# Performance work log

Measured on AMD Instinct MI355X. Metric: run time of the kernel, lower is better.

## Reference

```python
import jax, jax.numpy as jnp
import numpy as np

K = 3          # kernel size
STRIDE = 1
PAD = 1
GROUPS = 32    # GroupNorm groups
EPS = 1e-5


def setup_inputs() -> dict:
    key = jax.random.key(0)
    ks = jax.random.split(key, 6)
    B, Cin, H, W, Cout = 4, 256, 64, 64, 256
    K2 = K * K
    x = jax.random.normal(ks[0], (B, Cin, H, W), jnp.float32)
    offset = jax.random.normal(ks[1], (B, 2 * K2, H, W), jnp.float32)
    mask = jax.random.uniform(ks[2], (B, K2, H, W), jnp.float32)
    weight = jax.random.normal(ks[3], (Cout, Cin, K, K), jnp.float32) * (1.0 / np.sqrt(Cin * K2))
    bias = jnp.zeros((Cout,), jnp.float32)
    gamma = jnp.ones((Cout,), jnp.float32)   # constant_init(norm, 1)
    beta = jnp.zeros((Cout,), jnp.float32)   # bias=0
    return {"x": x, "offset": offset, "mask": mask, "weight": weight,
            "bias": bias, "gamma": gamma, "beta": beta}


def _modulated_deform_conv(x, offset, mask, weight, bias):
    """DCNv2: bilinear-sample x at learned offsets, modulate by mask, conv-accumulate."""
    B, Cin, H, W = x.shape
    Cout = weight.shape[0]
    K2 = K * K
    Ho = (H + 2 * PAD - K) // STRIDE + 1
    Wo = (W + 2 * PAD - K) // STRIDE + 1

    # base sampling grid per kernel point: [K2, Ho, Wo]
    ky, kx = jnp.meshgrid(jnp.arange(K), jnp.arange(K), indexing='ij')
    ky = ky.reshape(K2).astype(jnp.float32)
    kx = kx.reshape(K2).astype(jnp.float32)
    hs = (jnp.arange(Ho) * STRIDE - PAD).astype(jnp.float32)
    ws = (jnp.arange(Wo) * STRIDE - PAD).astype(jnp.float32)

    off = offset.reshape(B, K2, 2, Ho, Wo)  # interleaved (dy, dx) per kernel point
    y = ky[None, :, None, None] + hs[None, None, :, None] + off[:, :, 0]   # [B,K2,Ho,Wo]
    xc = kx[None, :, None, None] + ws[None, None, None, :] + off[:, :, 1]  # [B,K2,Ho,Wo]

    y0 = jnp.floor(y)
    x0 = jnp.floor(xc)
    dy = y - y0
    dx = xc - x0
    y0i = y0.astype(jnp.int32)
    x0i = x0.astype(jnp.int32)

    x_flat = x.reshape(B, Cin, H * W)

    def corner(yi, xi, w):
        # corner-wise zero padding outside the image (matches mmcv bilinear)
        valid = (yi >= 0) & (yi <= H - 1) & (xi >= 0) & (xi <= W - 1)
        idx = jnp.clip(yi, 0, H - 1) * W + jnp.clip(xi, 0, W - 1)  # [B,K2,Ho,Wo]
        idx_f = idx.reshape(B, -1)
        v = jax.vmap(lambda xf, i: xf[:, i])(x_flat, idx_f)  # [B, Cin, K2*Ho*Wo]
        wv = (w * valid.astype(w.dtype)).reshape(B, 1, -1)
        return v * wv

    val = (corner(y0i,     x0i,     (1 - dy) * (1 - dx))
         + corner(y0i,     x0i + 1, (1 - dy) * dx)
         + corner(y0i + 1, x0i,     dy * (1 - dx))
         + corner(y0i + 1, x0i + 1, dy * dx))
    val = val.reshape(B, Cin, K2, Ho, Wo) * mask[:, None]  # modulate

    w_r = weight.reshape(Cout, Cin, K2)
    out = jnp.einsum('bckhw,ock->bohw', val, w_r) + bias[None, :, None, None]
    return out


def _group_norm(x, gamma, beta):
    B, C, H, W = x.shape
    g = x.reshape(B, GROUPS, C // GROUPS, H, W)
    mu = g.mean(axis=(2, 3, 4), keepdims=True)
    var = ((g - mu) ** 2).mean(axis=(2, 3, 4), keepdims=True)
    g = (g - mu) * jax.lax.rsqrt(var + EPS)
    return g.reshape(B, C, H, W) * gamma[None, :, None, None] + beta[None, :, None, None]


def reference(x, offset, mask, weight, bias, gamma, beta):
    out = _modulated_deform_conv(x, offset, mask, weight, bias)
    out = _group_norm(out, gamma, beta)
    return jax.nn.relu(out)
```

## Files before the change

kernel.cpp:

```cpp
#include <hip/hip_runtime.h>
#include <math.h>

#define BB    4
#define CIN   256
#define HH    64
#define WWID  64
#define COUT  256
#define KKS   3
#define K2    9
#define PADV  1
#define HWSZ  4096
#define GROUPS 32
#define CPG   8
#define EPSV  1e-5f
#define ROWB  4608
#define NKC   36

typedef __attribute__((ext_vector_type(8))) short bf16x8;
typedef __attribute__((ext_vector_type(4))) float f32x4;

#define GLOAD_LDS16(g, l) \
    __builtin_amdgcn_global_load_lds((const __attribute__((address_space(1))) unsigned int*)(g), \
                                     (__attribute__((address_space(3))) unsigned int*)(l), 16, 0, 0)

__device__ __forceinline__ unsigned short f2bf(float f) {
    unsigned u = __float_as_uint(f);
    u = (u + 0x7fffu + ((u >> 16) & 1u)) >> 16;
    return (unsigned short)u;
}
__device__ __forceinline__ float bflo(unsigned q) { return __uint_as_float(q << 16); }
__device__ __forceinline__ float bfhi(unsigned q) { return __uint_as_float(q & 0xffff0000u); }
__device__ __forceinline__ void fma8(float* f, float w, uint4 q) {
    f[0] += w * bflo(q.x); f[1] += w * bfhi(q.x);
    f[2] += w * bflo(q.y); f[3] += w * bfhi(q.y);
    f[4] += w * bflo(q.z); f[5] += w * bfhi(q.z);
    f[6] += w * bflo(q.w); f[7] += w * bfhi(q.w);
}

__global__ __launch_bounds__(256)
void k_pre(const float* __restrict__ x, unsigned short* __restrict__ xh,
           const float* __restrict__ w, unsigned short* __restrict__ wtb,
           float* __restrict__ gstat) {
    int t = threadIdx.x;
    if (blockIdx.x < 128) {
        __shared__ float tile[32][33];
        int hw0 = blockIdx.x * 32;
        int c0  = blockIdx.y * 32;
        int b   = blockIdx.z;
        int tx = t & 31, ty = t >> 5;
        const float* xp = x + (size_t)b * CIN * HWSZ;
        #pragma unroll
        for (int i = 0; i < 4; i++)
            tile[ty + i * 8][tx] = xp[(c0 + ty + i * 8) * HWSZ + hw0 + tx];
        __syncthreads();
        int j = t >> 3, cq = t & 7;
        union { unsigned short s[4]; uint2 d; } pk;
        #pragma unroll
        for (int k = 0; k < 4; k++) pk.s[k] = f2bf(tile[cq * 4 + k][j]);
        *(uint2*)((char*)xh + ((size_t)b * HWSZ * CIN + (size_t)(hw0 + j) * CIN + c0 + cq * 4) * 2) = pk.d;
    } else {
        if (blockIdx.y == 0 && blockIdx.z == 0)
            for (int i = t; i < BB * GROUPS * 2 + 8; i += 256) gstat[i] = 0.f;
        int idx = (blockIdx.y * 4 + blockIdx.z) * 256 + t;
        int co = idx >> 5, c8 = idx & 31;
        int cin0 = c8 * 8;
        int q = c8 >> 3, c = c8 & 7;
        int pc = c ^ (co & 7);
        for (int k2 = 0; k2 < K2; k2++) {
            union { unsigned short s[8]; uint4 qq; } pk;
            #pragma unroll
            for (int j = 0; j < 8; j++)
                pk.s[j] = f2bf(w[(co * CIN + cin0 + j) * K2 + k2]);
            int phys = co * ROWB + k2 * 512 + q * 128 + pc * 16;
            *(uint4*)((char*)wtb + phys) = pk.qq;
        }
    }
}

__global__ __launch_bounds__(256)
void k_conv(const unsigned short* __restrict__ wtb, const unsigned short* __restrict__ xh,
            const float* __restrict__ offset, const float* __restrict__ mask,
            const float* __restrict__ bias, float* __restrict__ out,
            float* __restrict__ gstat) {
    __shared__ unsigned short As[128 * 64];
    __shared__ unsigned short Bs[64 * 64];
    __shared__ int   cidx[64 * K2 * 4];
    __shared__ float cwgt[64 * K2 * 4];
    __shared__ float gs[16], gss[16];

    int lid = blockIdx.x;
    int j8  = lid >> 3;
    int mt  = j8 & 1;
    int strip = (lid & 7) * 32 + (j8 >> 1);
    int b = strip >> 6;
    int hwbase = (strip & 63) * 64;
    int m0 = mt * 128;

    int t = threadIdx.x, w = t >> 6, l = t & 63;
    int r16 = l & 15, half = l >> 4;
    int wm = w & 1, wn = w >> 1;
    int skey = r16 & 7;

    if (t < 16) { gs[t] = 0.f; gss[t] = 0.f; }

    for (int i = t; i < 64 * K2; i += 256) {
        int px = i / K2, k2 = i - px * K2;
        int hw = hwbase + px;
        int ho = hw >> 6, wo = hw & 63;
        int ky = k2 / KKS, kx = k2 - ky * KKS;
        float dy = offset[((b * (2 * K2) + k2 * 2 + 0) * HWSZ) + hw];
        float dx = offset[((b * (2 * K2) + k2 * 2 + 1) * HWSZ) + hw];
        float m  = mask[(b * K2 + k2) * HWSZ + hw];
        float y  = (float)(ky + ho - PADV) + dy;
        float xc = (float)(kx + wo - PADV) + dx;
        float y0f = floorf(y), x0f = floorf(xc);
        float fy = y - y0f, fx = xc - x0f;
        int y0 = (int)y0f, x0 = (int)x0f;
        int   yy[2] = { y0, y0 + 1 };
        int   xx[2] = { x0, x0 + 1 };
        float wy[2] = { 1.f - fy, fy };
        float wx[2] = { 1.f - fx, fx };
        #pragma unroll
        for (int ii = 0; ii < 2; ii++)
            #pragma unroll
            for (int jj = 0; jj < 2; jj++) {
                int yi = yy[ii], xi = xx[jj];
                bool valid = (yi >= 0) && (yi < HH) && (xi >= 0) && (xi < WWID);
                int yc  = min(max(yi, 0), HH - 1);
                int xcc = min(max(xi, 0), WWID - 1);
                cidx[i * 4 + ii * 2 + jj] = yc * WWID + xcc;
                cwgt[i * 4 + ii * 2 + jj] = valid ? (wy[ii] * wx[jj] * m) : 0.f;
            }
    }

    const char* ag[4]; unsigned short* lA[4];
    #pragma unroll
    for (int i = 0; i < 4; i++) {
        int o = i * 256 + t;
        ag[i] = (const char*)wtb + (size_t)(m0 + (o >> 3)) * ROWB + (o & 7) * 16;
        lA[i] = (unsigned short*)As + o * 8;
    }

    int sc  = t & 7;
    int px0 = t >> 3;
    const char* xb = (const char*)xh + (size_t)b * HWSZ * CIN * 2;
    int bofs0 = px0 * 64 + (sc ^ (px0 & 7)) * 8;
    int px1 = px0 + 32;
    int bofs1 = px1 * 64 + (sc ^ (px1 & 7)) * 8;

    f32x4 acc[4][2];
    #pragma unroll
    for (int mi = 0; mi < 4; mi++)
        #pragma unroll
        for (int ni = 0; ni < 2; ni++) acc[mi][ni] = (f32x4)0.f;

    __syncthreads();

    uint4 g[2][4]; float gw[2][4];
    #pragma unroll
    for (int it = 0; it < 2; it++) {
        int cb = ((it ? px1 : px0) * K2) * 4;
        #pragma unroll
        for (int c = 0; c < 4; c++) {
            gw[it][c] = cwgt[cb + c];
            g[it][c]  = *(const uint4*)(xb + (size_t)cidx[cb + c] * 512 + sc * 16);
        }
    }

    for (int kc = 0; kc < NKC; kc++) {
        #pragma unroll
        for (int i = 0; i < 4; i++) { GLOAD_LDS16(ag[i], lA[i]); ag[i] += 128; }

        #pragma unroll
        for (int it = 0; it < 2; it++) {
            float f[8] = {0,0,0,0,0,0,0,0};
            fma8(f, gw[it][0], g[it][0]); fma8(f, gw[it][1], g[it][1]);
            fma8(f, gw[it][2], g[it][2]); fma8(f, gw[it][3], g[it][3]);
            union { unsigned short s[8]; uint4 qq; } pk;
            #pragma unroll
            for (int e = 0; e < 8; e++) pk.s[e] = f2bf(f[e]);
            *(uint4*)&Bs[it ? bofs1 : bofs0] = pk.qq;
        }
        __syncthreads();

        if (kc < NKC - 1) {
            int kn = kc + 1;
            int k2n = kn >> 2, qn = kn & 3;
            #pragma unroll
            for (int it = 0; it < 2; it++) {
                int cb = ((it ? px1 : px0) * K2 + k2n) * 4;
                #pragma unroll
                for (int c = 0; c < 4; c++) {
                    gw[it][c] = cwgt[cb + c];
                    g[it][c]  = *(const uint4*)(xb + (size_t)cidx[cb + c] * 512 + qn * 128 + sc * 16);
                }
            }
        }

        #pragma unroll
        for (int ks = 0; ks < 2; ks++) {
            int up = ((ks * 4 + half) ^ skey) * 8;
            bf16x8 af[4], bv[2];
            #pragma unroll
            for (int mi = 0; mi < 4; mi++)
                af[mi] = *(const bf16x8*)&As[(wm * 64 + mi * 16 + r16) * 64 + up];
            #pragma unroll
            for (int ni = 0; ni < 2; ni++)
                bv[ni] = *(const bf16x8*)&Bs[(wn * 32 + ni * 16 + r16) * 64 + up];
            #pragma unroll
            for (int mi = 0; mi < 4; mi++)
                #pragma unroll
                for (int ni = 0; ni < 2; ni++)
                    acc[mi][ni] = __builtin_amdgcn_mfma_f32_16x16x32_bf16(
                        af[mi], bv[ni], acc[mi][ni], 0, 0, 0);
        }
        __syncthreads();
    }

    float s4[4] = {0,0,0,0}, ss4[4] = {0,0,0,0};
    #pragma unroll
    for (int mi = 0; mi < 4; mi++) {
        #pragma unroll
        for (int r = 0; r < 4; r++) {
            int co = m0 + wm * 64 + mi * 16 + half * 4 + r;
            float bs = bias[co];
            float* orow = out + ((size_t)(b * COUT + co)) * HWSZ;
            #pragma unroll
            for (int ni = 0; ni < 2; ni++) {
                int n = hwbase + wn * 32 + ni * 16 + r16;
                float v = acc[mi][ni][r] + bs;
                orow[n] = v;
                s4[mi] += v; ss4[mi] += v * v;
            }
        }
    }
    int gb = half >> 1;
    #pragma unroll
    for (int mi = 0; mi < 4; mi++) {
        atomicAdd(&gs [wm * 8 + mi * 2 + gb], s4[mi]);
        atomicAdd(&gss[wm * 8 + mi * 2 + gb], ss4[mi]);
    }
    __syncthreads();
    if (t < 16) {
        int gidx = (m0 >> 3) + t;
        atomicAdd(&gstat[(b * GROUPS + gidx) * 2 + 0], gs[t]);
        atomicAdd(&gstat[(b * GROUPS + gidx) * 2 + 1], gss[t]);
    }
}

__global__ __launch_bounds__(256)
void k_gnfinal(float* __restrict__ out, const float* __restrict__ gstat,
               const float* __restrict__ gamma, const float* __restrict__ beta) {
    int i4 = blockIdx.x * 256 + threadIdx.x;
    int e  = i4 * 4;
    int c  = (e >> 12) & 255;
    int b  = e >> 20;
    int g  = c >> 3;
    float s  = gstat[((b * GROUPS) + g) * 2 + 0];
    float ss = gstat[((b * GROUPS) + g) * 2 + 1];
    const float inv = 1.f / (float)(CPG * HWSZ);
    float mu  = s * inv;
    float var = ss * inv - mu * mu;
    float rstd = rsqrtf(var + EPSV);
    float ga = gamma[c] * rstd;
    float be = beta[c] - mu * ga;
    float4 v = ((float4*)out)[i4];
    v.x = fmaxf(v.x * ga + be, 0.f);
    v.y = fmaxf(v.y * ga + be, 0.f);
    v.z = fmaxf(v.z * ga + be, 0.f);
    v.w = fmaxf(v.w * ga + be, 0.f);
    ((float4*)out)[i4] = v;
}

extern "C" void kernel_launch(void* const* d_in, const int* in_sizes, int n_in,
                              void* d_out, int out_size, void* d_ws, size_t ws_size,
                              hipStream_t stream) {
    const float* x      = (const float*)d_in[0];
    const float* offset = (const float*)d_in[1];
    const float* mask   = (const float*)d_in[2];
    const float* weight = (const float*)d_in[3];
    const float* bias   = (const float*)d_in[4];
    const float* gamma  = (const float*)d_in[5];
    const float* beta   = (const float*)d_in[6];
    float* out = (float*)d_out;

    unsigned short* xh    = (unsigned short*)d_ws;
    unsigned short* wtb   = xh + (size_t)4194304;
    float*          gstat = (float*)(wtb + (size_t)589824);

    k_pre<<<dim3(129, 8, 4), 256, 0, stream>>>(x, xh, weight, wtb, gstat);
    k_conv<<<512, 256, 0, stream>>>(wtb, xh, offset, mask, bias, out, gstat);
    k_gnfinal<<<(size_t)BB * COUT * HWSZ / 1024, 256, 0, stream>>>(out, gstat, gamma, beta);
}
```

Before: 151.3 us.

## Switch deformable conv to fp16 with packed-half bilinear gather and K=128 tiles

Converts the input and weight staging from bf16 to fp16 and uses fp16 MFMA. The bilinear interpolation now runs on packed half2 FMAs instead of unpacking bf16 to fp32 and repacking. The K chunk per iteration is doubled from 64 to 128 with a new LDS swizzle, which halves the loop trip count and the number of barriers. The cost is more LDS and register use, plus reduced precision because the interpolation is accumulated in fp16, where overflow and rounding can occur.

```diff
diff --git a/kernel.cpp b/kernel.cpp
--- a/kernel.cpp
+++ b/kernel.cpp
@@ -14,28 +14,22 @@
 #define CPG   8
 #define EPSV  1e-5f
 #define ROWB  4608
-#define NKC   36
-
-typedef __attribute__((ext_vector_type(8))) short bf16x8;
+#define NKC   18
+
+typedef __attribute__((ext_vector_type(8))) _Float16 f16x8;
+typedef __attribute__((ext_vector_type(2))) _Float16 h2;
 typedef __attribute__((ext_vector_type(4))) float f32x4;
 
 #define GLOAD_LDS16(g, l) \
     __builtin_amdgcn_global_load_lds((const __attribute__((address_space(1))) unsigned int*)(g), \
                                      (__attribute__((address_space(3))) unsigned int*)(l), 16, 0, 0)
 
-__device__ __forceinline__ unsigned short f2bf(float f) {
-    unsigned u = __float_as_uint(f);
-    u = (u + 0x7fffu + ((u >> 16) & 1u)) >> 16;
-    return (unsigned short)u;
-}
-__device__ __forceinline__ float bflo(unsigned q) { return __uint_as_float(q << 16); }
-__device__ __forceinline__ float bfhi(unsigned q) { return __uint_as_float(q & 0xffff0000u); }
-__device__ __forceinline__ void fma8(float* f, float w, uint4 q) {
-    f[0] += w * bflo(q.x); f[1] += w * bfhi(q.x);
-    f[2] += w * bflo(q.y); f[3] += w * bfhi(q.y);
-    f[4] += w * bflo(q.z); f[5] += w * bfhi(q.z);
-    f[6] += w * bflo(q.w); f[7] += w * bfhi(q.w);
-}
+__device__ __forceinline__ int physchunk(int c, int row) {
+    return ((c & 7) ^ (row & 7)) | ((c & 8) ^ ((row & 1) << 3));
+}
+
+union U4h { uint4 q; h2 h[4]; };
+union U1h { unsigned u; h2 h; };
 
 __global__ __launch_bounds__(256)
 void k_pre(const float* __restrict__ x, unsigned short* __restrict__ xh,
@@ -54,9 +48,9 @@
             tile[ty + i * 8][tx] = xp[(c0 + ty + i * 8) * HWSZ + hw0 + tx];
         __syncthreads();
         int j = t >> 3, cq = t & 7;
-        union { unsigned short s[4]; uint2 d; } pk;
-        #pragma unroll
-        for (int k = 0; k < 4; k++) pk.s[k] = f2bf(tile[cq * 4 + k][j]);
+        union { _Float16 h[4]; uint2 d; } pk;
+        #pragma unroll
+        for (int k = 0; k < 4; k++) pk.h[k] = (_Float16)tile[cq * 4 + k][j];
         *(uint2*)((char*)xh + ((size_t)b * HWSZ * CIN + (size_t)(hw0 + j) * CIN + c0 + cq * 4) * 2) = pk.d;
     } else {
         if (blockIdx.y == 0 && blockIdx.z == 0)
@@ -64,14 +58,14 @@
         int idx = (blockIdx.y * 4 + blockIdx.z) * 256 + t;
         int co = idx >> 5, c8 = idx & 31;
         int cin0 = c8 * 8;
-        int q = c8 >> 3, c = c8 & 7;
-        int pc = c ^ (co & 7);
+        int w2 = c8 >> 4, c = c8 & 15;
+        int pc = physchunk(c, co);
         for (int k2 = 0; k2 < K2; k2++) {
-            union { unsigned short s[8]; uint4 qq; } pk;
+            union { _Float16 h[8]; uint4 qq; } pk;
             #pragma unroll
             for (int j = 0; j < 8; j++)
-                pk.s[j] = f2bf(w[(co * CIN + cin0 + j) * K2 + k2]);
-            int phys = co * ROWB + k2 * 512 + q * 128 + pc * 16;
+                pk.h[j] = (_Float16)w[(co * CIN + cin0 + j) * K2 + k2];
+            int phys = co * ROWB + k2 * 512 + w2 * 256 + pc * 16;
             *(uint4*)((char*)wtb + phys) = pk.qq;
         }
     }
@@ -82,10 +76,10 @@
             const float* __restrict__ offset, const float* __restrict__ mask,
             const float* __restrict__ bias, float* __restrict__ out,
             float* __restrict__ gstat) {
-    __shared__ unsigned short As[128 * 64];
-    __shared__ unsigned short Bs[64 * 64];
-    __shared__ int   cidx[64 * K2 * 4];
-    __shared__ float cwgt[64 * K2 * 4];
+    __shared__ unsigned short As[128 * 128];
+    __shared__ unsigned short Bs[64 * 128];
+    __shared__ int      cidx[64 * K2 * 4];
+    __shared__ unsigned cwgt[64 * K2 * 4];
     __shared__ float gs[16], gss[16];
 
     int lid = blockIdx.x;
@@ -99,7 +93,6 @@
     int t = threadIdx.x, w = t >> 6, l = t & 63;
     int r16 = l & 15, half = l >> 4;
     int wm = w & 1, wn = w >> 1;
-    int skey = r16 & 7;
 
     if (t < 16) { gs[t] = 0.f; gss[t] = 0.f; }
 
@@ -129,24 +122,26 @@
                 int yc  = min(max(yi, 0), HH - 1);
                 int xcc = min(max(xi, 0), WWID - 1);
                 cidx[i * 4 + ii * 2 + jj] = yc * WWID + xcc;
-                cwgt[i * 4 + ii * 2 + jj] = valid ? (wy[ii] * wx[jj] * m) : 0.f;
-            }
-    }
-
-    const char* ag[4]; unsigned short* lA[4];
-    #pragma unroll
-    for (int i = 0; i < 4; i++) {
-        int o = i * 256 + t;
-        ag[i] = (const char*)wtb + (size_t)(m0 + (o >> 3)) * ROWB + (o & 7) * 16;
-        lA[i] = (unsigned short*)As + o * 8;
-    }
-
-    int sc  = t & 7;
-    int px0 = t >> 3;
+                float wv = valid ? (wy[ii] * wx[jj] * m) : 0.f;
+                U1h cw; cw.h = h2{(_Float16)wv, (_Float16)wv};
+                cwgt[i * 4 + ii * 2 + jj] = cw.u;
+            }
+    }
+
+    const char* ag[8]; unsigned short* lA[8];
+    #pragma unroll
+    for (int i = 0; i < 8; i++) {
+        int o = (w * 8 + i) * 64 + l;
+        ag[i] = (const char*)wtb + (size_t)(m0 + (o >> 4)) * ROWB + (o & 15) * 16;
+        lA[i] = (unsigned short*)As + (w * 8 + i) * 512;
+    }
+
+    int spx = t >> 2, sq = t & 3;
     const char* xb = (const char*)xh + (size_t)b * HWSZ * CIN * 2;
-    int bofs0 = px0 * 64 + (sc ^ (px0 & 7)) * 8;
-    int px1 = px0 + 32;
-    int bofs1 = px1 * 64 + (sc ^ (px1 & 7)) * 8;
+    int bq[4];
+    #pragma unroll
+    for (int j = 0; j < 4; j++)
+        bq[j] = spx * 128 + physchunk(sq * 4 + j, spx) * 8;
 
     f32x4 acc[4][2];
     #pragma unroll
@@ -156,62 +151,67 @@
 
     __syncthreads();
 
-    uint4 g[2][4]; float gw[2][4];
-    #pragma unroll
-    for (int it = 0; it < 2; it++) {
-        int cb = ((it ? px1 : px0) * K2) * 4;
+    uint4 g[4][4]; h2 gw[4];
+    {
+        int cb = (spx * K2) * 4;
         #pragma unroll
         for (int c = 0; c < 4; c++) {
-            gw[it][c] = cwgt[cb + c];
-            g[it][c]  = *(const uint4*)(xb + (size_t)cidx[cb + c] * 512 + sc * 16);
+            U1h cw; cw.u = cwgt[cb + c]; gw[c] = cw.h;
+            const char* p = xb + (size_t)cidx[cb + c] * 512 + sq * 64;
+            #pragma unroll
+            for (int j = 0; j < 4; j++) g[c][j] = *(const uint4*)(p + j * 16);
         }
     }
 
     for (int kc = 0; kc < NKC; kc++) {
         #pragma unroll
-        for (int i = 0; i < 4; i++) { GLOAD_LDS16(ag[i], lA[i]); ag[i] += 128; }
-
-        #pragma unroll
-        for (int it = 0; it < 2; it++) {
-            float f[8] = {0,0,0,0,0,0,0,0};
-            fma8(f, gw[it][0], g[it][0]); fma8(f, gw[it][1], g[it][1]);
-            fma8(f, gw[it][2], g[it][2]); fma8(f, gw[it][3], g[it][3]);
-            union { unsigned short s[8]; uint4 qq; } pk;
-            #pragma unroll
-            for (int e = 0; e < 8; e++) pk.s[e] = f2bf(f[e]);
-            *(uint4*)&Bs[it ? bofs1 : bofs0] = pk.qq;
+        for (int i = 0; i < 8; i++) { GLOAD_LDS16(ag[i], lA[i]); ag[i] += 256; }
+
+        #pragma unroll
+        for (int j = 0; j < 4; j++) {
+            h2 a0 = h2{0, 0}, a1 = h2{0, 0}, a2 = h2{0, 0}, a3 = h2{0, 0};
+            #pragma unroll
+            for (int c = 0; c < 4; c++) {
+                U4h xv; xv.q = g[c][j];
+                a0 = gw[c] * xv.h[0] + a0;
+                a1 = gw[c] * xv.h[1] + a1;
+                a2 = gw[c] * xv.h[2] + a2;
+                a3 = gw[c] * xv.h[3] + a3;
+            }
+            U4h o; o.h[0] = a0; o.h[1] = a1; o.h[2] = a2; o.h[3] = a3;
+            *(uint4*)&Bs[bq[j]] = o.q;
         }
         __syncthreads();
 
         if (kc < NKC - 1) {
             int kn = kc + 1;
-            int k2n = kn >> 2, qn = kn & 3;
-            #pragma unroll
-            for (int it = 0; it < 2; it++) {
-                int cb = ((it ? px1 : px0) * K2 + k2n) * 4;
+            int k2n = kn >> 1, hs = kn & 1;
+            int cb = (spx * K2 + k2n) * 4;
+            #pragma unroll
+            for (int c = 0; c < 4; c++) {
+                U1h cw; cw.u = cwgt[cb + c]; gw[c] = cw.h;
+                const char* p = xb + (size_t)cidx[cb + c] * 512 + hs * 256 + sq * 64;
                 #pragma unroll
-                for (int c = 0; c < 4; c++) {
-                    gw[it][c] = cwgt[cb + c];
-                    g[it][c]  = *(const uint4*)(xb + (size_t)cidx[cb + c] * 512 + qn * 128 + sc * 16);
-                }
-            }
-        }
-
-        #pragma unroll
-        for (int ks = 0; ks < 2; ks++) {
-            int up = ((ks * 4 + half) ^ skey) * 8;
-            bf16x8 af[4], bv[2];
+                for (int j = 0; j < 4; j++) g[c][j] = *(const uint4*)(p + j * 16);
+            }
+        }
+
+        #pragma unroll
+        for (int ks = 0; ks < 4; ks++) {
+            int ks4 = ks * 4 + half;
+            int up  = physchunk(ks4, r16) * 8;
+            f16x8 af[4], bv[2];
             #pragma unroll
             for (int mi = 0; mi < 4; mi++)
-                af[mi] = *(const bf16x8*)&As[(wm * 64 + mi * 16 + r16) * 64 + up];
+                af[mi] = *(const f16x8*)&As[(wm * 64 + mi * 16 + r16) * 128 + up];
             #pragma unroll
             for (int ni = 0; ni < 2; ni++)
-                bv[ni] = *(const bf16x8*)&Bs[(wn * 32 + ni * 16 + r16) * 64 + up];
+                bv[ni] = *(const f16x8*)&Bs[(wn * 32 + ni * 16 + r16) * 128 + up];
             #pragma unroll
             for (int mi = 0; mi < 4; mi++)
                 #pragma unroll
                 for (int ni = 0; ni < 2; ni++)
-                    acc[mi][ni] = __builtin_amdgcn_mfma_f32_16x16x32_bf16(
+                    acc[mi][ni] = __builtin_amdgcn_mfma_f32_16x16x32_f16(
                         af[mi], bv[ni], acc[mi][ni], 0, 0, 0);
         }
         __syncthreads();
```

Result: slower. 160.4 us (+6.0%).
